# Performance work log

Hardware: AMD Instinct MI355X
Metric: run time of the kernel (lower is better)

Reference implementation:

```python
import jax, jax.numpy as jnp
import numpy as np

B, T, HID = 2, 2048, 2048
NH, NKV = 16, 8
NOPE, ROPE = 128, 64
HD = NOPE + ROPE  # 192
VD = 128
KV_RANK, Q_RANK = 512, 1536
EPS = 1e-6
THETA = 10000.0
GROUPS = NH // NKV


def rmsnorm(x, w):
    var = jnp.mean(x * x, axis=-1, keepdims=True)
    return x * jax.lax.rsqrt(var + EPS) * w


def rope_cos_sin(seq_len, dtype):
    inv_freq = 1.0 / (THETA ** (jnp.arange(0, ROPE, 2, dtype=jnp.float32) / ROPE))
    t = jnp.arange(seq_len, dtype=jnp.float32)
    freqs = jnp.outer(t, inv_freq)
    emb = jnp.concatenate([freqs, freqs], axis=-1)  # [T, ROPE]
    return jnp.cos(emb).astype(dtype)[None, :, None, :], jnp.sin(emb).astype(dtype)[None, :, None, :]


def rotate_half(x):
    x1, x2 = x[..., : x.shape[-1] // 2], x[..., x.shape[-1] // 2 :]
    return jnp.concatenate([-x2, x1], axis=-1)


def setup_inputs() -> dict:
    key = jax.random.key(0)
    ks = jax.random.split(key, 7)
    s = 0.02
    return {
        "hidden_states": jax.random.normal(ks[0], (B, T, HID), jnp.float32),
        "q_a_w": jax.random.normal(ks[1], (HID, Q_RANK), jnp.float32) * s,
        "q_a_ln_w": jnp.ones((Q_RANK,), jnp.float32),
        "q_b_w": jax.random.normal(ks[2], (Q_RANK, NH * HD), jnp.float32) * s,
        "kv_a_w": jax.random.normal(ks[3], (HID, KV_RANK + NKV * ROPE), jnp.float32) * s,
        "kv_a_ln_w": jnp.ones((KV_RANK,), jnp.float32),
        "kv_b_w": jax.random.normal(ks[4], (KV_RANK, NKV * (NOPE + VD)), jnp.float32) * s,
        "o_w": jax.random.normal(ks[5], (NH * VD, HID), jnp.float32) * s,
    }


def reference(hidden_states, q_a_w, q_a_ln_w, q_b_w, kv_a_w, kv_a_ln_w, kv_b_w, o_w):
    x = hidden_states
    # Q low-rank path: a_proj -> RMSNorm -> b_proj
    q = rmsnorm(x @ q_a_w, q_a_ln_w) @ q_b_w
    q = q.reshape(B, T, NH, HD)
    q_nope, q_rope = q[..., :NOPE], q[..., NOPE:]
    # KV low-rank + decoupled rope key
    kv_raw = x @ kv_a_w
    kv_latent = rmsnorm(kv_raw[..., :KV_RANK], kv_a_ln_w)
    k_rope = kv_raw[..., KV_RANK:].reshape(B, T, NKV, ROPE)
    kv = (kv_latent @ kv_b_w).reshape(B, T, NKV, NOPE + VD)
    k_nope, v = kv[..., :NOPE], kv[..., NOPE:]
    # partial RoPE on rope slice only
    cos, sin = rope_cos_sin(T, x.dtype)
    q_rope = q_rope * cos + rotate_half(q_rope) * sin
    k_rope = k_rope * cos + rotate_half(k_rope) * sin
    q_full = jnp.concatenate([q_nope, q_rope], axis=-1)  # [B,T,NH,HD]
    k_full = jnp.concatenate([k_nope, k_rope], axis=-1)  # [B,T,NKV,HD]
    # GQA expansion (repeat_interleave over head dim)
    k_full = jnp.repeat(k_full, GROUPS, axis=2)  # [B,T,NH,HD]
    v_full = jnp.repeat(v, GROUPS, axis=2)       # [B,T,NH,VD]
    scale = HD ** -0.5
    scores = jnp.einsum("bqhd,bkhd->bhqk", q_full, k_full) * scale
    probs = jax.nn.softmax(scores, axis=-1)
    attn = jnp.einsum("bhqk,bkhd->bqhd", probs, v_full)
    out = attn.reshape(B, T, NH * VD) @ o_w
    return out
```

## Files before the change

### kernel.cpp

```cpp
#include <hip/hip_runtime.h>

using u16 = unsigned short;
using u32 = unsigned int;

typedef float f32x4 __attribute__((ext_vector_type(4)));
typedef __bf16 bf16x8 __attribute__((ext_vector_type(8)));

__device__ __forceinline__ u16 f2bf(float f){
  u32 u = __builtin_bit_cast(u32, f);
  u32 r = (u + 0x7fffu + ((u >> 16) & 1u)) >> 16;
  return (u16)r;
}
__device__ __forceinline__ float bf2f(u16 h){
  u32 u = ((u32)h) << 16;
  return __builtin_bit_cast(float, u);
}
__device__ __forceinline__ void gl2lds16(const void* g, void* l){
  __builtin_amdgcn_global_load_lds((const __attribute__((address_space(1))) u32*)g,
                                   (__attribute__((address_space(3))) u32*)l, 16, 0, 0);
}
__device__ __forceinline__ int swz24(int ck, int r){ return (ck & 24) | ((ck ^ r) & 7); }
__device__ __forceinline__ u32 cvtpk_bf16(float a, float b){
  u32 r; asm("v_cvt_pk_bf16_f32 %0, %1, %2" : "=v"(r) : "v"(a), "v"(b)); return r;
}

__global__ __launch_bounds__(256) void cvt_f32_bf16(const float* __restrict__ in,
                                                    u16* __restrict__ out, long n){
  long i = ((long)blockIdx.x*256 + threadIdx.x)*4;
  if (i >= n) return;
  float4 v = *(const float4*)(in + i);
  u16 o[4] = { f2bf(v.x), f2bf(v.y), f2bf(v.z), f2bf(v.w) };
  *(ushort4*)(out + i) = *(ushort4*)o;
}

__global__ __launch_bounds__(256) void transpose_w(const float* __restrict__ in,
                                                   u16* __restrict__ out, int K, int N){
  __shared__ float tile[32][33];
  int n0 = blockIdx.x*32, k0 = blockIdx.y*32;
  int tx = threadIdx.x, ty = threadIdx.y;
  for (int i = ty; i < 32; i += 8)
    tile[i][tx] = in[(size_t)(k0+i)*N + n0+tx];
  __syncthreads();
  for (int i = ty; i < 32; i += 8)
    out[(size_t)(n0+i)*K + k0+tx] = f2bf(tile[tx][i]);
}

__global__ __launch_bounds__(256) void rope_tables(float* __restrict__ cosT, float* __restrict__ sinT){
  int idx = blockIdx.x*256 + threadIdx.x;
  int t = idx >> 5, d = idx & 31;
  double inv = pow(10000.0, -(double)d / 32.0);
  double a = (double)t * inv;
  cosT[idx] = (float)cos(a);
  sinT[idx] = (float)sin(a);
}

template<int OUT_BF16>
__global__ __launch_bounds__(256) void gemm_bt(const u16* __restrict__ A,
                                               const u16* __restrict__ Bt,
                                               void* __restrict__ Cout,
                                               int M, int N, int K, float cscale){
  __shared__ u16 As[128*32];
  __shared__ u16 Bs[128*32];
  const int tid = threadIdx.x, lane = tid & 63, wave = tid >> 6;
  const int m0 = blockIdx.y*128, n0 = blockIdx.x*128;
  const int wm = (wave >> 1)*64, wn = (wave & 1)*64;
  const int g = lane >> 4, lr = lane & 15;
  f32x4 acc[4][4] = {};
  const int sr = (wave*2)*16 + (lane >> 2);
  const int sc = (lane & 3)*8;
  for (int k0 = 0; k0 < K; k0 += 32){
    __syncthreads();
    #pragma unroll
    for (int i = 0; i < 2; i++){
      int c = wave*2 + i;
      int r = sr + i*16;
      gl2lds16(A  + (size_t)(m0+r)*K + k0 + sc, (char*)As + c*1024);
      gl2lds16(Bt + (size_t)(n0+r)*K + k0 + sc, (char*)Bs + c*1024);
    }
    __syncthreads();
    bf16x8 af[4], bfr[4];
    #pragma unroll
    for (int mi = 0; mi < 4; mi++) af[mi]  = *reinterpret_cast<const bf16x8*>(&As[(wm+mi*16+lr)*32 + g*8]);
    #pragma unroll
    for (int ni = 0; ni < 4; ni++) bfr[ni] = *reinterpret_cast<const bf16x8*>(&Bs[(wn+ni*16+lr)*32 + g*8]);
    #pragma unroll
    for (int mi = 0; mi < 4; mi++)
      #pragma unroll
      for (int ni = 0; ni < 4; ni++)
        acc[mi][ni] = __builtin_amdgcn_mfma_f32_16x16x32_bf16(af[mi], bfr[ni], acc[mi][ni], 0,0,0);
  }
  #pragma unroll
  for (int mi = 0; mi < 4; mi++)
    #pragma unroll
    for (int ni = 0; ni < 4; ni++)
      #pragma unroll
      for (int r = 0; r < 4; r++){
        int row = m0 + wm + mi*16 + g*4 + r;
        int col = n0 + wn + ni*16 + lr;
        float v = acc[mi][ni][r];
        if (OUT_BF16) ((u16*)Cout)[(size_t)row*N + col] = f2bf(v*cscale);
        else          ((float*)Cout)[(size_t)row*N + col] = v;
      }
}

__global__ __launch_bounds__(256) void rmsnorm_kernel(const float* __restrict__ in,
                                                      const float* __restrict__ w,
                                                      u16* __restrict__ out, int ncols, int instride){
  int row = blockIdx.x;
  const float* x = in + (size_t)row*instride;
  float ss = 0.f;
  for (int c = threadIdx.x; c < ncols; c += 256){ float v = x[c]; ss += v*v; }
  #pragma unroll
  for (int m = 1; m < 64; m <<= 1) ss += __shfl_xor(ss, m, 64);
  __shared__ float p[4];
  if ((threadIdx.x & 63) == 0) p[threadIdx.x >> 6] = ss;
  __syncthreads();
  float inv = rsqrtf((p[0]+p[1]+p[2]+p[3]) / (float)ncols + 1e-6f);
  u16* o = out + (size_t)row*ncols;
  for (int c = threadIdx.x; c < ncols; c += 256) o[c] = f2bf(x[c]*inv*w[c]);
}

__global__ __launch_bounds__(256) void kv_split_kernel(const float* __restrict__ kvraw,
                                                       const float* __restrict__ lnw,
                                                       const float* __restrict__ cosT,
                                                       const float* __restrict__ sinT,
                                                       u16* __restrict__ kvlat,
                                                       u16* __restrict__ Kf){
  int row = blockIdx.x;
  int t = row & 2047, b = row >> 11;
  const float* x = kvraw + (size_t)row*2560 + 1536;
  float ss = 0.f;
  for (int c = threadIdx.x; c < 512; c += 256){ float v = x[c]; ss += v*v; }
  #pragma unroll
  for (int m = 1; m < 64; m <<= 1) ss += __shfl_xor(ss, m, 64);
  __shared__ float p[4];
  if ((threadIdx.x & 63) == 0) p[threadIdx.x >> 6] = ss;
  __syncthreads();
  float inv = rsqrtf((p[0]+p[1]+p[2]+p[3]) / 512.0f + 1e-6f);
  for (int c = threadIdx.x; c < 512; c += 256)
    kvlat[(size_t)row*512 + c] = f2bf(x[c]*inv*lnw[c]);
  int kh = threadIdx.x >> 5, dp = threadIdx.x & 31;
  float x1 = x[512 + kh*64 + dp], x2 = x[512 + kh*64 + dp + 32];
  float cv = cosT[t*32 + dp], sv = sinT[t*32 + dp];
  float o1 = x1*cv - x2*sv;
  float o2 = x2*cv + x1*sv;
  u16* kr = Kf + ((size_t)(b*8 + kh)*2048 + t)*192;
  int c1 = 128 + dp, c2 = 128 + dp + 32;
  kr[(swz24(c1 >> 3, t) << 3) | (c1 & 7)] = f2bf(o1);
  kr[(swz24(c2 >> 3, t) << 3) | (c2 & 7)] = f2bf(o2);
}

__global__ __launch_bounds__(256) void q_rope_kernel(u16* __restrict__ q,
                                                     const float* __restrict__ cosT,
                                                     const float* __restrict__ sinT){
  int idx = blockIdx.x*256 + threadIdx.x;
  int row = idx >> 9, rem = idx & 511;
  int h = rem >> 5, dp = rem & 31;
  int t = row & 2047;
  u16* pq = q + (size_t)row*3072 + h*192 + 128;
  float x1 = bf2f(pq[dp]), x2 = bf2f(pq[dp+32]);
  float cv = cosT[t*32 + dp], sv = sinT[t*32 + dp];
  pq[dp]    = f2bf(x1*cv - x2*sv);
  pq[dp+32] = f2bf(x2*cv + x1*sv);
}

__global__ __launch_bounds__(256) void knope_kernel(const u16* __restrict__ kv,
                                                    u16* __restrict__ Kf){
  int idx = blockIdx.x*256 + threadIdx.x;
  int row = idx >> 7, rem = idx & 127;
  int kh = rem >> 4, ck = rem & 15;
  int t = row & 2047, b = row >> 11;
  int ck2 = (ck & 8) | ((ck ^ t) & 7);
  uint4 v = *(const uint4*)(kv + (size_t)row*2048 + kh*256 + ck*8);
  *(uint4*)(Kf + ((size_t)(b*8 + kh)*2048 + t)*192 + ck2*8) = v;
}

__global__ __launch_bounds__(256) void v_transpose(const u16* __restrict__ kv,
                                                   u16* __restrict__ vT){
  int bid = blockIdx.x;
  int tt = bid & 31, kvh = (bid >> 5) & 7, b = bid >> 8;
  int t0 = tt*64;
  __shared__ u16 tile[64][136];
  int tid = threadIdx.x;
  #pragma unroll
  for (int i = 0; i < 4; i++){
    int c = tid + i*256;
    int r = c >> 4, ck = c & 15;
    const u16* src = kv + ((size_t)(b*2048 + t0 + r))*2048 + kvh*256 + 128 + ck*8;
    *(uint4*)&tile[r][ck*8] = *(const uint4*)src;
  }
  __syncthreads();
  #pragma unroll
  for (int i = 0; i < 4; i++){
    int c = tid + i*256;
    int vd = c >> 3, tc = c & 7;
    int stc = tc ^ (vd & 7);
    uint4 tv;
    u16* tp = (u16*)&tv;
    #pragma unroll
    for (int j = 0; j < 8; j++) tp[j] = tile[tc*8 + j][vd];
    *(uint4*)(vT + ((size_t)(b*8 + kvh)*128 + vd)*2048 + t0 + stc*8) = tv;
  }
}

__global__ __launch_bounds__(256, 2) void attn_kernel(const u16* __restrict__ Q,
                                                      const u16* __restrict__ Kf,
                                                      const u16* __restrict__ Vt,
                                                      u16* __restrict__ Oa){
  constexpr int T = 2048;
  constexpr int NT = T/64;
  __shared__ u16 Ks[64*192];
  __shared__ u16 Vs[2][128*64];
  __shared__ u16 Ps[4][2048];
  const int tid = threadIdx.x, lane = tid & 63, wave = tid >> 6;
  const int g = lane >> 4, lr = lane & 15;

  const int wg = blockIdx.x;
  const int role = (wg & 7)*64 + (wg >> 3);
  const int grp = role >> 5;
  const int b = grp >> 3, kvh = grp & 7;
  const int within = role & 31;
  const int h = kvh*2 + (within >> 4);
  const int q0 = (within & 15)*128 + wave*32;

  bf16x8 aq[2][6];
  #pragma unroll
  for (int qg = 0; qg < 2; qg++){
    const u16* qrow = Q + ((size_t)b*T + q0 + qg*16 + lr)*3072 + h*192;
    #pragma unroll
    for (int kc = 0; kc < 6; kc++)
      aq[qg][kc] = *reinterpret_cast<const bf16x8*>(qrow + kc*32 + g*8);
  }
  const u16* Kbase = Kf + (size_t)(b*8 + kvh)*T*192;
  const u16* Vbase = Vt + (size_t)(b*8 + kvh)*128*T;

  f32x4 ovb[2][8] = {};
  float mq[2] = {-1e30f, -1e30f};
  float lq[2] = {0.f, 0.f};

  auto stageK = [&](int kt){
    const u16* ksrc = Kbase + (size_t)kt*12288 + wave*3072 + lane*8;
    #pragma unroll
    for (int i = 0; i < 6; i++)
      gl2lds16(ksrc + i*512, (char*)Ks + (wave*6 + i)*1024);
  };
  auto stageV = [&](int kt, int buf){
    #pragma unroll
    for (int i = 0; i < 4; i++){
      int c = wave*4 + i;
      const u16* vsrc = Vbase + (size_t)(c*8 + (lane >> 3))*T + kt*64 + (lane & 7)*8;
      gl2lds16(vsrc, (char*)(&Vs[0][0]) + buf*16384 + c*1024);
    }
  };

  stageK(0);
  stageV(0, 0);
  __syncthreads();

  int buf = 0;
  for (int kt = 0; kt < NT; kt++){
    const bool notlast = (kt + 1 < NT);

    if (notlast) stageV(kt + 1, buf ^ 1);

    f32x4 s[2][4];
    __builtin_amdgcn_s_setprio(1);
    #pragma unroll
    for (int nb = 0; nb < 4; nb++){
      const int row = nb*16 + lr;
      f32x4 a0 = {0.f,0.f,0.f,0.f}, a1 = {0.f,0.f,0.f,0.f};
      #pragma unroll
      for (int kc = 0; kc < 6; kc++){
        int ckl = swz24(kc*4 + g, row);
        bf16x8 kf = *reinterpret_cast<const bf16x8*>(&Ks[row*192 + ckl*8]);
        a0 = __builtin_amdgcn_mfma_f32_16x16x32_bf16(kf, aq[0][kc], a0, 0,0,0);
        a1 = __builtin_amdgcn_mfma_f32_16x16x32_bf16(kf, aq[1][kc], a1, 0,0,0);
      }
      s[0][nb] = a0; s[1][nb] = a1;
    }
    __builtin_amdgcn_s_setprio(0);

    asm volatile("s_waitcnt lgkmcnt(0)" ::: "memory");
    __builtin_amdgcn_s_barrier();
    __builtin_amdgcn_sched_barrier(0);
    if (notlast) stageK(kt + 1);

    #pragma unroll
    for (int qg = 0; qg < 2; qg++){
      float pm = s[qg][0][0];
      #pragma unroll
      for (int nb = 0; nb < 4; nb++)
        #pragma unroll
        for (int r = 0; r < 4; r++)
          if (nb || r) pm = fmaxf(pm, s[qg][nb][r]);
      pm = fmaxf(pm, __shfl_xor(pm, 16, 64));
      pm = fmaxf(pm, __shfl_xor(pm, 32, 64));
      if (!__all(pm <= mq[qg] + 8.f)){
        float mn = fmaxf(mq[qg], pm);
        float corr = __expf(mq[qg] - mn);
        mq[qg] = mn;
        lq[qg] *= corr;
        #pragma unroll
        for (int r = 0; r < 4; r++){
          float cr = __shfl(corr, (lane & 48) | (g*4 + r), 64);
          #pragma unroll
          for (int vb = 0; vb < 8; vb++) ovb[qg][vb][r] *= cr;
        }
      }
      float ls = 0.f;
      #pragma unroll
      for (int nb = 0; nb < 4; nb++){
        float e0 = __expf(s[qg][nb][0] - mq[qg]);
        float e1 = __expf(s[qg][nb][1] - mq[qg]);
        float e2 = __expf(s[qg][nb][2] - mq[qg]);
        float e3 = __expf(s[qg][nb][3] - mq[qg]);
        ls += (e0 + e1) + (e2 + e3);
        int stc = (2*nb + (g >> 1)) ^ (lr & 7);
        volatile u32* p = (volatile u32*)&Ps[wave][qg*1024 + lr*64 + stc*8 + (g & 1)*4];
        p[0] = cvtpk_bf16(e0, e1);
        p[1] = cvtpk_bf16(e2, e3);
      }
      ls += __shfl_xor(ls, 16, 64);
      ls += __shfl_xor(ls, 32, 64);
      lq[qg] += ls;
    }

    asm volatile("s_waitcnt lgkmcnt(0)" ::: "memory");
    __builtin_amdgcn_sched_barrier(0);

    bf16x8 ap[2][2];
    #pragma unroll
    for (int qg = 0; qg < 2; qg++)
      #pragma unroll
      for (int k2 = 0; k2 < 2; k2++){
        int ck = (k2*4 + g) ^ (lr & 7);
        ap[qg][k2] = *reinterpret_cast<const bf16x8*>(&Ps[wave][qg*1024 + lr*64 + ck*8]);
      }
    __builtin_amdgcn_s_setprio(1);
    #pragma unroll
    for (int vb = 0; vb < 8; vb++)
      #pragma unroll
      for (int k2 = 0; k2 < 2; k2++){
        int vd = vb*16 + lr;
        int ck = (k2*4 + g) ^ (vd & 7);
        bf16x8 bv = *reinterpret_cast<const bf16x8*>(&Vs[buf][vd*64 + ck*8]);
        ovb[0][vb] = __builtin_amdgcn_mfma_f32_16x16x32_bf16(ap[0][k2], bv, ovb[0][vb], 0,0,0);
        ovb[1][vb] = __builtin_amdgcn_mfma_f32_16x16x32_bf16(ap[1][k2], bv, ovb[1][vb], 0,0,0);
      }
    __builtin_amdgcn_s_setprio(0);

    if (notlast) __syncthreads();
    buf ^= 1;
  }

  #pragma unroll
  for (int qg = 0; qg < 2; qg++){
    float invq = 1.0f / lq[qg];
    float inv_r[4];
    #pragma unroll
    for (int r = 0; r < 4; r++)
      inv_r[r] = __shfl(invq, (lane & 48) | (g*4 + r), 64);
    u16* obase = Oa + ((size_t)b*T + q0 + qg*16)*2048 + h*128;
    #pragma unroll
    for (int vb = 0; vb < 8; vb++)
      #pragma unroll
      for (int r = 0; r < 4; r++)
        obase[(size_t)(g*4 + r)*2048 + vb*16 + lr] = f2bf(ovb[qg][vb][r]*inv_r[r]);
  }
}

extern "C" void kernel_launch(void* const* d_in, const int* in_sizes, int n_in,
                              void* d_out, int out_size, void* d_ws, size_t ws_size,
                              hipStream_t stream){
  const float* hs      = (const float*)d_in[0];
  const float* q_a_w   = (const float*)d_in[1];
  const float* q_a_ln  = (const float*)d_in[2];
  const float* q_b_w   = (const float*)d_in[3];
  const float* kv_a_w  = (const float*)d_in[4];
  const float* kv_a_ln = (const float*)d_in[5];
  const float* kv_b_w  = (const float*)d_in[6];
  const float* o_w     = (const float*)d_in[7];

  char* ws = (char*)d_ws;
  size_t off = 0;
  auto alloc = [&](size_t bytes){ void* p = ws + off; off += bytes; return p; };
  u16*  Wqa   = (u16*)alloc(1536ull*2048*2);
  u16*  Wkva  = (u16*)alloc(1024ull*2048*2);
  u16*  Wqb   = (u16*)alloc(3072ull*1536*2);
  u16*  Wkvb  = (u16*)alloc(2048ull*512*2);
  u16*  Wo    = (u16*)alloc(2048ull*2048*2);
  u16*  XB    = (u16*)alloc(4096ull*2048*2);
  char* R23   = (char*)alloc(4096ull*2560*4);
  u16*  Qlat  = (u16*)alloc(4096ull*1536*2);
  u16*  KVlat = (u16*)alloc(4096ull*512*2);
  u16*  Kf    = (u16*)alloc(2ull*8*2048*192*2);
  u16*  Vt    = (u16*)alloc(2ull*8*128*2048*2);
  float* cosT = (float*)alloc(2048ull*32*4);
  float* sinT = (float*)alloc(2048ull*32*4);
  (void)ws_size; (void)in_sizes; (void)n_in; (void)out_size;

  u16* QB  = (u16*)R23;
  u16* KVB = (u16*)(R23 + 4096ull*3072*2);

  const float qscale = 0.07216878364870322f;

  cvt_f32_bf16<<<8192, 256, 0, stream>>>(hs, XB, 4096ll*2048);
  transpose_w<<<dim3(1536/32, 2048/32), dim3(32,8), 0, stream>>>(q_a_w,  Wqa,  2048, 1536);
  transpose_w<<<dim3(1024/32, 2048/32), dim3(32,8), 0, stream>>>(kv_a_w, Wkva, 2048, 1024);
  transpose_w<<<dim3(3072/32, 1536/32), dim3(32,8), 0, stream>>>(q_b_w,  Wqb,  1536, 3072);
  transpose_w<<<dim3(2048/32,  512/32), dim3(32,8), 0, stream>>>(kv_b_w, Wkvb,  512, 2048);
  transpose_w<<<dim3(2048/32, 2048/32), dim3(32,8), 0, stream>>>(o_w,    Wo,   2048, 2048);
  rope_tables<<<256, 256, 0, stream>>>(cosT, sinT);

  gemm_bt<0><<<dim3(20, 32), 256, 0, stream>>>(XB, Wqa, (float*)R23, 4096, 2560, 2048, 1.0f);
  rmsnorm_kernel<<<4096, 256, 0, stream>>>((const float*)R23, q_a_ln, Qlat, 1536, 2560);
  kv_split_kernel<<<4096, 256, 0, stream>>>((const float*)R23, kv_a_ln, cosT, sinT, KVlat, Kf);
  gemm_bt<1><<<dim3(24, 32), 256, 0, stream>>>(Qlat, Wqb, QB, 4096, 3072, 1536, qscale);
  q_rope_kernel<<<8192, 256, 0, stream>>>(QB, cosT, sinT);
  gemm_bt<1><<<dim3(16, 32), 256, 0, stream>>>(KVlat, Wkvb, KVB, 4096, 2048, 512, 1.0f);
  knope_kernel<<<2048, 256, 0, stream>>>(KVB, Kf);
  v_transpose<<<512, 256, 0, stream>>>(KVB, Vt);
  attn_kernel<<<512, 256, 0, stream>>>(QB, Kf, Vt, XB);
  gemm_bt<0><<<dim3(16, 32), 256, 0, stream>>>(XB, Wo, (float*)d_out, 4096, 2048, 2048, 1.0f);
}
```

Baseline: 371.4 us.

## Fuse Q rope into GEMM, bf16 intermediates, merge KV rearrange, swizzle GEMM blocks

Moves Q RoPE into the epilogue of the q_b GEMM and merges the k_nope copy with the V transpose into one kernel, so two launches and one pass over the Q and KV tensors go away. The first projection now writes bf16 instead of fp32, which halves that intermediate's traffic, and the rmsnorm and kv_split kernels use vectorized bf16 loads. GEMM blocks get a grouped remap of block IDs meant to improve L2 reuse. The cost is that the pre-norm activations are rounded to bf16 before RMSNorm. The remap hardcodes 32 row blocks, which matches every grid launched here.

Result: faster. 348.5 us (-6.2%).

```diff
diff --git a/kernel.cpp b/kernel.cpp
--- a/kernel.cpp
+++ b/kernel.cpp
@@ -54,6 +54,12 @@
   sinT[idx] = (float)sin(a);
 }
 
+__device__ __forceinline__ void remap_block(int NX, int& bx, int& by){
+  int id = blockIdx.y*NX + blockIdx.x;
+  bx = id >> 5;
+  by = ((id & 7) << 2) | ((id >> 3) & 3);
+}
+
 template<int OUT_BF16>
 __global__ __launch_bounds__(256) void gemm_bt(const u16* __restrict__ A,
                                                const u16* __restrict__ Bt,
@@ -62,7 +68,8 @@
   __shared__ u16 As[128*32];
   __shared__ u16 Bs[128*32];
   const int tid = threadIdx.x, lane = tid & 63, wave = tid >> 6;
-  const int m0 = blockIdx.y*128, n0 = blockIdx.x*128;
+  int bx, by; remap_block(gridDim.x, bx, by);
+  const int m0 = by*128, n0 = bx*128;
   const int wm = (wave >> 1)*64, wn = (wave & 1)*64;
   const int g = lane >> 4, lr = lane & 15;
   f32x4 acc[4][4] = {};
@@ -103,24 +110,101 @@
       }
 }
 
-__global__ __launch_bounds__(256) void rmsnorm_kernel(const float* __restrict__ in,
-                                                      const float* __restrict__ w,
-                                                      u16* __restrict__ out, int ncols, int instride){
+__global__ __launch_bounds__(256) void gemm_qb_rope(const u16* __restrict__ A,
+                                                    const u16* __restrict__ Bt,
+                                                    u16* __restrict__ C,
+                                                    const float* __restrict__ cosT,
+                                                    const float* __restrict__ sinT){
+  constexpr int N = 3072, K = 1536;
+  constexpr float qscale = 0.07216878364870322f;
+  __shared__ u16 As[128*32];
+  __shared__ u16 Bs[128*32];
+  const int tid = threadIdx.x, lane = tid & 63, wave = tid >> 6;
+  int bx, by; remap_block(gridDim.x, bx, by);
+  const int m0 = by*128, n0 = bx*128;
+  const int wm = (wave >> 1)*64, wn = (wave & 1)*64;
+  const int g = lane >> 4, lr = lane & 15;
+  f32x4 acc[4][4] = {};
+  const int sr = (wave*2)*16 + (lane >> 2);
+  const int sc = (lane & 3)*8;
+  for (int k0 = 0; k0 < K; k0 += 32){
+    __syncthreads();
+    #pragma unroll
+    for (int i = 0; i < 2; i++){
+      int c = wave*2 + i;
+      int r = sr + i*16;
+      gl2lds16(A  + (size_t)(m0+r)*K + k0 + sc, (char*)As + c*1024);
+      gl2lds16(Bt + (size_t)(n0+r)*K + k0 + sc, (char*)Bs + c*1024);
+    }
+    __syncthreads();
+    bf16x8 af[4], bfr[4];
+    #pragma unroll
+    for (int mi = 0; mi < 4; mi++) af[mi]  = *reinterpret_cast<const bf16x8*>(&As[(wm+mi*16+lr)*32 + g*8]);
+    #pragma unroll
+    for (int ni = 0; ni < 4; ni++) bfr[ni] = *reinterpret_cast<const bf16x8*>(&Bs[(wn+ni*16+lr)*32 + g*8]);
+    #pragma unroll
+    for (int mi = 0; mi < 4; mi++)
+      #pragma unroll
+      for (int ni = 0; ni < 4; ni++)
+        acc[mi][ni] = __builtin_amdgcn_mfma_f32_16x16x32_bf16(af[mi], bfr[ni], acc[mi][ni], 0,0,0);
+  }
+  const bool rope = (((n0 + wn) >> 6) % 3) == 2;
+  #pragma unroll
+  for (int mi = 0; mi < 4; mi++)
+    #pragma unroll
+    for (int r = 0; r < 4; r++){
+      int row = m0 + wm + mi*16 + g*4 + r;
+      int t = row & 2047;
+      u16* crow = C + (size_t)row*N + n0 + wn;
+      if (rope){
+        #pragma unroll
+        for (int np = 0; np < 2; np++){
+          int dp = np*16 + lr;
+          float x1 = acc[mi][np][r]*qscale, x2 = acc[mi][np+2][r]*qscale;
+          float cv = cosT[t*32 + dp], sv = sinT[t*32 + dp];
+          crow[dp]      = f2bf(x1*cv - x2*sv);
+          crow[dp + 32] = f2bf(x2*cv + x1*sv);
+        }
+      } else {
+        #pragma unroll
+        for (int ni = 0; ni < 4; ni++)
+          crow[ni*16 + lr] = f2bf(acc[mi][ni][r]*qscale);
+      }
+    }
+}
+
+__global__ __launch_bounds__(256) void rmsnorm_bf16(const u16* __restrict__ in,
+                                                    const float* __restrict__ w,
+                                                    u16* __restrict__ out, int ncols, int instride){
   int row = blockIdx.x;
-  const float* x = in + (size_t)row*instride;
+  const u16* x = in + (size_t)row*instride;
+  int c = threadIdx.x;
+  float xs[8];
   float ss = 0.f;
-  for (int c = threadIdx.x; c < ncols; c += 256){ float v = x[c]; ss += v*v; }
+  int nch = ncols >> 3;
+  if (c < nch){
+    ushort4 a = *(const ushort4*)(x + c*8);
+    ushort4 bq = *(const ushort4*)(x + c*8 + 4);
+    u16 e[8] = {a.x,a.y,a.z,a.w,bq.x,bq.y,bq.z,bq.w};
+    #pragma unroll
+    for (int j = 0; j < 8; j++){ xs[j] = bf2f(e[j]); ss += xs[j]*xs[j]; }
+  }
   #pragma unroll
   for (int m = 1; m < 64; m <<= 1) ss += __shfl_xor(ss, m, 64);
   __shared__ float p[4];
   if ((threadIdx.x & 63) == 0) p[threadIdx.x >> 6] = ss;
   __syncthreads();
   float inv = rsqrtf((p[0]+p[1]+p[2]+p[3]) / (float)ncols + 1e-6f);
-  u16* o = out + (size_t)row*ncols;
-  for (int c = threadIdx.x; c < ncols; c += 256) o[c] = f2bf(x[c]*inv*w[c]);
-}
-
-__global__ __launch_bounds__(256) void kv_split_kernel(const float* __restrict__ kvraw,
+  if (c < nch){
+    u16 o[8];
+    #pragma unroll
+    for (int j = 0; j < 8; j++) o[j] = f2bf(xs[j]*inv*w[c*8+j]);
+    *(ushort4*)(out + (size_t)row*ncols + c*8)     = *(ushort4*)o;
+    *(ushort4*)(out + (size_t)row*ncols + c*8 + 4) = *(ushort4*)(o+4);
+  }
+}
+
+__global__ __launch_bounds__(256) void kv_split_kernel(const u16* __restrict__ kvraw,
                                                        const float* __restrict__ lnw,
                                                        const float* __restrict__ cosT,
                                                        const float* __restrict__ sinT,
@@ -128,19 +212,30 @@
                                                        u16* __restrict__ Kf){
   int row = blockIdx.x;
   int t = row & 2047, b = row >> 11;
-  const float* x = kvraw + (size_t)row*2560 + 1536;
+  const u16* x = kvraw + (size_t)row*2560 + 1536;
+  int c = threadIdx.x;
+  float xs[4];
   float ss = 0.f;
-  for (int c = threadIdx.x; c < 512; c += 256){ float v = x[c]; ss += v*v; }
+  if (c < 128){
+    ushort4 a = *(const ushort4*)(x + c*4);
+    u16 e[4] = {a.x,a.y,a.z,a.w};
+    #pragma unroll
+    for (int j = 0; j < 4; j++){ xs[j] = bf2f(e[j]); ss += xs[j]*xs[j]; }
+  }
   #pragma unroll
   for (int m = 1; m < 64; m <<= 1) ss += __shfl_xor(ss, m, 64);
   __shared__ float p[4];
   if ((threadIdx.x & 63) == 0) p[threadIdx.x >> 6] = ss;
   __syncthreads();
   float inv = rsqrtf((p[0]+p[1]+p[2]+p[3]) / 512.0f + 1e-6f);
-  for (int c = threadIdx.x; c < 512; c += 256)
-    kvlat[(size_t)row*512 + c] = f2bf(x[c]*inv*lnw[c]);
+  if (c < 128){
+    u16 o[4];
+    #pragma unroll
+    for (int j = 0; j < 4; j++) o[j] = f2bf(xs[j]*inv*lnw[c*4+j]);
+    *(ushort4*)(kvlat + (size_t)row*512 + c*4) = *(ushort4*)o;
+  }
   int kh = threadIdx.x >> 5, dp = threadIdx.x & 31;
-  float x1 = x[512 + kh*64 + dp], x2 = x[512 + kh*64 + dp + 32];
+  float x1 = bf2f(x[512 + kh*64 + dp]), x2 = bf2f(x[512 + kh*64 + dp + 32]);
   float cv = cosT[t*32 + dp], sv = sinT[t*32 + dp];
   float o1 = x1*cv - x2*sv;
   float o2 = x2*cv + x1*sv;
@@ -150,38 +245,23 @@
   kr[(swz24(c2 >> 3, t) << 3) | (c2 & 7)] = f2bf(o2);
 }
 
-__global__ __launch_bounds__(256) void q_rope_kernel(u16* __restrict__ q,
-                                                     const float* __restrict__ cosT,
-                                                     const float* __restrict__ sinT){
-  int idx = blockIdx.x*256 + threadIdx.x;
-  int row = idx >> 9, rem = idx & 511;
-  int h = rem >> 5, dp = rem & 31;
-  int t = row & 2047;
-  u16* pq = q + (size_t)row*3072 + h*192 + 128;
-  float x1 = bf2f(pq[dp]), x2 = bf2f(pq[dp+32]);
-  float cv = cosT[t*32 + dp], sv = sinT[t*32 + dp];
-  pq[dp]    = f2bf(x1*cv - x2*sv);
-  pq[dp+32] = f2bf(x2*cv + x1*sv);
-}
-
-__global__ __launch_bounds__(256) void knope_kernel(const u16* __restrict__ kv,
+__global__ __launch_bounds__(256) void kv_rearrange(const u16* __restrict__ kv,
+                                                    u16* __restrict__ vT,
                                                     u16* __restrict__ Kf){
-  int idx = blockIdx.x*256 + threadIdx.x;
-  int row = idx >> 7, rem = idx & 127;
-  int kh = rem >> 4, ck = rem & 15;
-  int t = row & 2047, b = row >> 11;
-  int ck2 = (ck & 8) | ((ck ^ t) & 7);
-  uint4 v = *(const uint4*)(kv + (size_t)row*2048 + kh*256 + ck*8);
-  *(uint4*)(Kf + ((size_t)(b*8 + kh)*2048 + t)*192 + ck2*8) = v;
-}
-
-__global__ __launch_bounds__(256) void v_transpose(const u16* __restrict__ kv,
-                                                   u16* __restrict__ vT){
   int bid = blockIdx.x;
   int tt = bid & 31, kvh = (bid >> 5) & 7, b = bid >> 8;
   int t0 = tt*64;
   __shared__ u16 tile[64][136];
   int tid = threadIdx.x;
+  #pragma unroll
+  for (int i = 0; i < 4; i++){
+    int c2 = tid + i*256;
+    int rr = c2 >> 4, ck = c2 & 15;
+    int t = t0 + rr;
+    int ck2 = (ck & 8) | ((ck ^ t) & 7);
+    uint4 v = *(const uint4*)(kv + ((size_t)(b*2048 + t))*2048 + kvh*256 + ck*8);
+    *(uint4*)(Kf + ((size_t)(b*8 + kvh)*2048 + t)*192 + ck2*8) = v;
+  }
   #pragma unroll
   for (int i = 0; i < 4; i++){
     int c = tid + i*256;
@@ -260,7 +340,6 @@
   int buf = 0;
   for (int kt = 0; kt < NT; kt++){
     const bool notlast = (kt + 1 < NT);
-
     if (notlast) stageV(kt + 1, buf ^ 1);
 
     f32x4 s[2][4];
@@ -390,7 +469,8 @@
   u16*  Wkvb  = (u16*)alloc(2048ull*512*2);
   u16*  Wo    = (u16*)alloc(2048ull*2048*2);
   u16*  XB    = (u16*)alloc(4096ull*2048*2);
-  char* R23   = (char*)alloc(4096ull*2560*4);
+  u16*  R23   = (u16*)alloc(4096ull*2560*2);
+  u16*  QB    = (u16*)alloc(4096ull*3072*2);
   u16*  Qlat  = (u16*)alloc(4096ull*1536*2);
   u16*  KVlat = (u16*)alloc(4096ull*512*2);
   u16*  Kf    = (u16*)alloc(2ull*8*2048*192*2);
@@ -399,10 +479,7 @@
   float* sinT = (float*)alloc(2048ull*32*4);
   (void)ws_size; (void)in_sizes; (void)n_in; (void)out_size;
 
-  u16* QB  = (u16*)R23;
-  u16* KVB = (u16*)(R23 + 4096ull*3072*2);
-
-  const float qscale = 0.07216878364870322f;
+  u16* KVB = R23;
 
   cvt_f32_bf16<<<8192, 256, 0, stream>>>(hs, XB, 4096ll*2048);
   transpose_w<<<dim3(1536/32, 2048/32), dim3(32,8), 0, stream>>>(q_a_w,  Wqa,  2048, 1536);
@@ -412,14 +489,12 @@
   transpose_w<<<dim3(2048/32, 2048/32), dim3(32,8), 0, stream>>>(o_w,    Wo,   2048, 2048);
   rope_tables<<<256, 256, 0, stream>>>(cosT, sinT);
 
-  gemm_bt<0><<<dim3(20, 32), 256, 0, stream>>>(XB, Wqa, (float*)R23, 4096, 2560, 2048, 1.0f);
-  rmsnorm_kernel<<<4096, 256, 0, stream>>>((const float*)R23, q_a_ln, Qlat, 1536, 2560);
-  kv_split_kernel<<<4096, 256, 0, stream>>>((const float*)R23, kv_a_ln, cosT, sinT, KVlat, Kf);
-  gemm_bt<1><<<dim3(24, 32), 256, 0, stream>>>(Qlat, Wqb, QB, 4096, 3072, 1536, qscale);
-  q_rope_kernel<<<8192, 256, 0, stream>>>(QB, cosT, sinT);
+  gemm_bt<1><<<dim3(20, 32), 256, 0, stream>>>(XB, Wqa, R23, 4096, 2560, 2048, 1.0f);
+  rmsnorm_bf16<<<4096, 256, 0, stream>>>(R23, q_a_ln, Qlat, 1536, 2560);
+  kv_split_kernel<<<4096, 256, 0, stream>>>(R23, kv_a_ln, cosT, sinT, KVlat, Kf);
+  gemm_qb_rope<<<dim3(24, 32), 256, 0, stream>>>(Qlat, Wqb, QB, cosT, sinT);
   gemm_bt<1><<<dim3(16, 32), 256, 0, stream>>>(KVlat, Wkvb, KVB, 4096, 2048, 512, 1.0f);
-  knope_kernel<<<2048, 256, 0, stream>>>(KVB, Kf);
-  v_transpose<<<512, 256, 0, stream>>>(KVB, Vt);
+  kv_rearrange<<<512, 256, 0, stream>>>(KVB, Vt, Kf);
   attn_kernel<<<512, 256, 0, stream>>>(QB, Kf, Vt, XB);
   gemm_bt<0><<<dim3(16, 32), 256, 0, stream>>>(XB, Wo, (float*)d_out, 4096, 2048, 2048, 1.0f);
 }
```
